# Kernel tuning notes

Measured on AMD Instinct MI355X. Metric: run time of the kernel, lower is better.

The kernel has to match this reference:

```python
import jax, jax.numpy as jnp
import numpy as np

B, CIN, COUT, H, W = 8, 64, 64, 56, 56
HEAD, KATT, KCONV = 1, 5, 3
HEAD_DIM = COUT // HEAD
PAD = (1 * (KATT - 1) + 1) // 2  # dilation=1 -> 2


def setup_inputs() -> dict:
    key = jax.random.key(0)
    ks = jax.random.split(key, 12)
    n = jax.random.normal
    return {
        'x': n(ks[0], (B, CIN, H, W), jnp.float32),
        'w1': n(ks[1], (COUT, CIN), jnp.float32) * 0.05,
        'b1': n(ks[2], (COUT,), jnp.float32) * 0.05,
        'w2': n(ks[3], (COUT, CIN), jnp.float32) * 0.05,
        'b2': n(ks[4], (COUT,), jnp.float32) * 0.05,
        'w3': n(ks[5], (COUT, CIN), jnp.float32) * 0.05,
        'b3': n(ks[6], (COUT,), jnp.float32) * 0.05,
        'wp': n(ks[7], (HEAD_DIM, 2), jnp.float32) * 0.05,
        'bp': n(ks[8], (HEAD_DIM,), jnp.float32) * 0.05,
        'w_fc': n(ks[9], (KCONV * KCONV, 3 * HEAD), jnp.float32) * 0.05,
        'w_dep': n(ks[10], (COUT, KCONV * KCONV, KCONV, KCONV), jnp.float32) * 0.05,
        'b_dep': n(ks[11], (COUT,), jnp.float32) * 0.05,
        'rate1': jnp.full((1,), 0.5, jnp.float32),
        'rate2': jnp.full((1,), 0.5, jnp.float32),
    }


def _conv1x1(x, w, b):
    return jnp.einsum('oc,bchw->bohw', w, x) + b[None, :, None, None]


def _unfold(x, h, w):
    # reflection-pad then extract KATTxKATT patches -> (n, c, KATT*KATT, h, w)
    p = jnp.pad(x, ((0, 0), (0, 0), (PAD, PAD), (PAD, PAD)), mode='reflect')
    return jnp.stack([p[:, :, i:i + h, j:j + w]
                      for i in range(KATT) for j in range(KATT)], axis=2)


def reference(x, w1, b1, w2, b2, w3, b3, wp, bp, w_fc, w_dep, b_dep, rate1, rate2):
    b, _, h, w = x.shape
    q = _conv1x1(x, w1, b1)
    k = _conv1x1(x, w2, b2)
    v = _conv1x1(x, w3, b3)
    head_dim = wp.shape[0]
    head = q.shape[1] // head_dim
    scaling = float(head_dim) ** -0.5

    # relative position embedding (stride=1 so q_pe == pe)
    loc_w = jnp.tile(jnp.linspace(-1.0, 1.0, w)[None, :], (h, 1))
    loc_h = jnp.tile(jnp.linspace(-1.0, 1.0, h)[:, None], (1, w))
    pe = _conv1x1(jnp.stack([loc_w, loc_h])[None], wp, bp)  # (1, head_dim, h, w)

    q_att = q.reshape(b * head, head_dim, h, w) * scaling
    k_att = k.reshape(b * head, head_dim, h, w)
    v_att = v.reshape(b * head, head_dim, h, w)

    unfold_k = _unfold(k_att, h, w)          # (b*head, d, 25, h, w)
    unfold_rpe = _unfold(pe, h, w)           # (1, d, 25, h, w)
    att = jnp.sum(q_att[:, :, None] * (unfold_k + pe[:, :, None] - unfold_rpe), axis=1)
    att = jax.nn.softmax(att, axis=1)        # softmax over the 25 window positions
    unfold_v = _unfold(v_att, h, w)
    out_att = jnp.sum(att[:, None] * unfold_v, axis=2).reshape(b, -1, h, w)

    # parallel depthwise-conv branch
    f_cat = jnp.concatenate([q.reshape(b, head, head_dim, h * w),
                             k.reshape(b, head, head_dim, h * w),
                             v.reshape(b, head, head_dim, h * w)], axis=1)  # (b, 3h, d, hw)
    f_all = jnp.einsum('oc,bcdl->bodl', w_fc, f_cat)                        # (b, 9, d, hw)
    f_conv = jnp.transpose(f_all, (0, 2, 1, 3)).reshape(b, head_dim * KCONV * KCONV, h, w)
    out_conv = jax.lax.conv_general_dilated(
        f_conv, w_dep, window_strides=(1, 1), padding=((1, 1), (1, 1)),
        feature_group_count=head_dim,
        dimension_numbers=('NCHW', 'OIHW', 'NCHW')) + b_dep[None, :, None, None]

    return rate1[0] * out_att + rate2[0] * out_conv
```

## Files before the change

kernel.cpp:

```cpp
#include <hip/hip_runtime.h>

#define HH 56
#define WWID 56
#define HWP (HH*WWID)
#define BB 8
#define CC 64
#define NPIX (BB*HWP)

__device__ __forceinline__ float grp_sum(float x) {
  int xi;
  xi = __builtin_amdgcn_update_dpp(0, __float_as_int(x), 0xB1, 0xF, 0xF, true);
  x += __int_as_float(xi);
  xi = __builtin_amdgcn_update_dpp(0, __float_as_int(x), 0x4E, 0xF, 0xF, true);
  x += __int_as_float(xi);
  xi = __builtin_amdgcn_update_dpp(0, __float_as_int(x), 0x141, 0xF, 0xF, true);
  x += __int_as_float(xi);
  xi = __builtin_amdgcn_update_dpp(0, __float_as_int(x), 0x140, 0xF, 0xF, true);
  x += __int_as_float(xi);
  return x;
}

__device__ __forceinline__ float dot4(float4 a, float4 b) {
  float t = a.x * b.x;
  t = fmaf(a.y, b.y, t);
  t = fmaf(a.z, b.z, t);
  t = fmaf(a.w, b.w, t);
  return t;
}

__device__ __forceinline__ float fcomp(const float4 v, int i) {
  return i == 0 ? v.x : i == 1 ? v.y : i == 2 ? v.z : v.w;
}

__global__ __launch_bounds__(256) void prep_kernel(
    const float* __restrict__ w1, const float* __restrict__ w2, const float* __restrict__ w3,
    const float* __restrict__ w_fc, const float* __restrict__ w_dep,
    float* __restrict__ w1P, float* __restrict__ w2P, float* __restrict__ w3P,
    float* __restrict__ tab)
{
  const int gt = blockIdx.x * 256 + threadIdx.x;
  {
    const int idx = gt;
    const int c4 = idx >> 8, r = idx & 255, o = r >> 2, e = r & 3;
    const int c = c4*4 + e;
    w1P[idx] = w1[o*64 + c];
    w2P[idx] = w2[o*64 + c];
    w3P[idx] = w3[o*64 + c];
  }
  if (gt < 27*64) {
    const int d = gt & 63, bt = gt >> 6;
    const int br = bt / 9, tap = bt - br*9;
    float s = 0.f;
    #pragma unroll
    for (int oo = 0; oo < 9; ++oo)
      s += w_dep[d*81 + oo*9 + tap] * w_fc[oo*3 + br];
    tab[gt] = s;
  }
}

__global__ __launch_bounds__(256) void qkv_kernel(
    const float* __restrict__ x,
    const float* __restrict__ b1, const float* __restrict__ b2, const float* __restrict__ b3,
    const float* __restrict__ w1P, const float* __restrict__ w2P, const float* __restrict__ w3P,
    float* __restrict__ q, float* __restrict__ k, float* __restrict__ v)
{
  __shared__ float xs[64 * 32];
  const int tid = threadIdx.x;

  int bid = (int)blockIdx.x;
  bid = (bid & 7) * 98 + (bid >> 3);

  const int pix0 = bid * 32;
  const int n    = pix0 / HWP;
  const int hw0  = pix0 - n * HWP;
  const float* xb = x + (size_t)n * CC * HWP + hw0;

  #pragma unroll
  for (int r = 0; r < 2; ++r) {
    int idx = r * 256 + tid;
    int c   = idx >> 3;
    int p4  = (idx & 7) * 4;
    *reinterpret_cast<float4*>(&xs[c*32 + p4]) =
        *reinterpret_cast<const float4*>(xb + (size_t)c * HWP + p4);
  }
  __syncthreads();

  const int o = tid & 63;
  const int g = __builtin_amdgcn_readfirstlane((int)(tid >> 6));
  const float* xg = &xs[g * 8];

  float accq[8], acck[8], accv[8];
  const float bq = b1[o], bk = b2[o], bv = b3[o];
  #pragma unroll
  for (int p = 0; p < 8; ++p) { accq[p] = bq; acck[p] = bk; accv[p] = bv; }

  float4 xbuf[2][4];
  float4 wqb[2], wkb[2], wvb[2];

  xbuf[0][0] = *reinterpret_cast<const float4*>(xg + 0*32);
  xbuf[0][1] = *reinterpret_cast<const float4*>(xg + 0*32 + 4);
  xbuf[0][2] = *reinterpret_cast<const float4*>(xg + 1*32);
  xbuf[0][3] = *reinterpret_cast<const float4*>(xg + 1*32 + 4);
  wqb[0] = *reinterpret_cast<const float4*>(w1P + o*4);
  wkb[0] = *reinterpret_cast<const float4*>(w2P + o*4);
  wvb[0] = *reinterpret_cast<const float4*>(w3P + o*4);

  #pragma unroll
  for (int ph = 0; ph < 32; ++ph) {
    const int cur  = ph & 1, nxt = cur ^ 1;
    const int c4   = ph >> 1;
    const int wsel = c4 & 1;
    if (ph < 31) {
      const int cn = (ph + 1) * 2;
      xbuf[nxt][0] = *reinterpret_cast<const float4*>(xg + (cn+0)*32);
      xbuf[nxt][1] = *reinterpret_cast<const float4*>(xg + (cn+0)*32 + 4);
      xbuf[nxt][2] = *reinterpret_cast<const float4*>(xg + (cn+1)*32);
      xbuf[nxt][3] = *reinterpret_cast<const float4*>(xg + (cn+1)*32 + 4);
    }
    if (cur == 0 && c4 < 15) {
      wqb[wsel^1] = *reinterpret_cast<const float4*>(w1P + (c4+1)*256 + o*4);
      wkb[wsel^1] = *reinterpret_cast<const float4*>(w2P + (c4+1)*256 + o*4);
      wvb[wsel^1] = *reinterpret_cast<const float4*>(w3P + (c4+1)*256 + o*4);
    }
    const float wq0 = fcomp(wqb[wsel], cur*2), wq1 = fcomp(wqb[wsel], cur*2+1);
    const float wk0 = fcomp(wkb[wsel], cur*2), wk1 = fcomp(wkb[wsel], cur*2+1);
    const float wv0 = fcomp(wvb[wsel], cur*2), wv1 = fcomp(wvb[wsel], cur*2+1);
    #pragma unroll
    for (int p = 0; p < 8; ++p) {
      const float x0 = (p < 4) ? fcomp(xbuf[cur][0], p) : fcomp(xbuf[cur][1], p-4);
      const float x1 = (p < 4) ? fcomp(xbuf[cur][2], p) : fcomp(xbuf[cur][3], p-4);
      accq[p] = fmaf(wq0, x0, accq[p]);
      acck[p] = fmaf(wk0, x0, acck[p]);
      accv[p] = fmaf(wv0, x0, accv[p]);
      accq[p] = fmaf(wq1, x1, accq[p]);
      acck[p] = fmaf(wk1, x1, acck[p]);
      accv[p] = fmaf(wv1, x1, accv[p]);
    }
  }

  const int pbase = pix0 + g * 8;
  #pragma unroll
  for (int p = 0; p < 8; ++p) {
    size_t off = (size_t)(pbase + p) * 64 + o;
    q[off] = accq[p]; k[off] = acck[p]; v[off] = accv[p];
  }
}

__global__ __launch_bounds__(256) void attn_kernel(
    const float* __restrict__ q, const float* __restrict__ k, const float* __restrict__ v,
    const float* __restrict__ wp, const float* __restrict__ tab,
    const float* __restrict__ b_dep, const float* __restrict__ rate1, const float* __restrict__ rate2,
    float* __restrict__ out)
{
  __shared__ float stab[27 * 64];
  __shared__ float sbd[64];
  __shared__ float sout[64 * 17];

  const int tid  = threadIdx.x;
  for (int i = tid; i < 27*64; i += 256) stab[i] = tab[i];
  if (tid < 64) sbd[tid] = b_dep[tid];
  __syncthreads();

  const int lane = tid & 63;
  const int wid  = __builtin_amdgcn_readfirstlane((int)(tid >> 6));
  const int grp  = lane >> 4;
  const int sl   = lane & 15;

  int bid = (int)blockIdx.x;
  bid = (bid & 7) * 196 + (bid >> 3);

  const int pixbase = bid * 16;
  const int pl  = wid * 4 + grp;
  const int pix = pixbase + pl;
  const int n   = pix / HWP;
  const int hw  = pix - n * HWP;
  const int h   = hw / WWID;
  const int w   = hw - h * WWID;

  const size_t nbase = (size_t)n * HWP * 64;
  const float4 q4 = *reinterpret_cast<const float4*>(q + nbase + (size_t)hw * 64 + sl * 4);

  int hr[5], wr[5];
  #pragma unroll
  for (int i = 0; i < 5; ++i) {
    int t = h + i - 2; hr[i] = t < 0 ? -t : (t >= HH ? 2*HH - 2 - t : t);
    t = w + i - 2;     wr[i] = t < 0 ? -t : (t >= WWID ? 2*WWID - 2 - t : t);
  }

  const float* kb = k + nbase + sl * 4;
  const float* vb = v + nbase + sl * 4;

  float4 ka[5], va[5];
  {
    const size_t rowoff = (size_t)(hr[0] * WWID) * 64;
    const float* krow = kb + rowoff;
    const float* vrow = vb + rowoff;
    #pragma unroll
    for (int j = 0; j < 5; ++j) ka[j] = *reinterpret_cast<const float4*>(krow + wr[j] * 64);
    #pragma unroll
    for (int j = 0; j < 5; ++j) va[j] = *reinterpret_cast<const float4*>(vrow + wr[j] * 64);
  }

  const float4 wa = *reinterpret_cast<const float4*>(wp + 8 * sl);
  const float4 wb = *reinterpret_cast<const float4*>(wp + 8 * sl + 4);
  const float4 wpx4 = {wa.x, wa.z, wb.x, wb.z};
  const float4 wpy4 = {wa.y, wa.w, wb.y, wb.w};
  const float qw0 = grp_sum(dot4(q4, wpx4));
  const float qw1 = grp_sum(dot4(q4, wpy4));

  const float LOG2E = 1.44269504f;
  const float L  = 0.125f * LOG2E;
  const float C  = 2.0f / 55.0f;
  const float A0 = L * qw0 * C;
  const float A1 = L * qw1 * C;

  float s = 0.f;
  float4 oatt = {0.f, 0.f, 0.f, 0.f};
  float4 cacc = {0.f, 0.f, 0.f, 0.f};

  #pragma unroll
  for (int i = 0; i < 5; ++i) {
    float4 kn[5], vn[5];
    if (i < 4) {
      const size_t rowoff = (size_t)(hr[i+1] * WWID) * 64;
      const float* krow = kb + rowoff;
      const float* vrow = vb + rowoff;
      #pragma unroll
      for (int j = 0; j < 5; ++j) kn[j] = *reinterpret_cast<const float4*>(krow + wr[j] * 64);
      #pragma unroll
      for (int j = 0; j < 5; ++j) vn[j] = *reinterpret_cast<const float4*>(vrow + wr[j] * 64);
    }

    const float rh = A1 * (float)(h - hr[i]);
    #pragma unroll
    for (int j = 0; j < 5; ++j) {
      const float d16 = grp_sum(dot4(q4, ka[j]));
      const float att = fmaf(L, d16, fmaf(A0, (float)(w - wr[j]), rh));
      const float p = __builtin_exp2f(att);
      s += p;
      oatt.x = fmaf(p, va[j].x, oatt.x);
      oatt.y = fmaf(p, va[j].y, oatt.y);
      oatt.z = fmaf(p, va[j].z, oatt.z);
      oatt.w = fmaf(p, va[j].w, oatt.w);
    }

    if (i >= 1 && i <= 3) {
      const int hh = h + i - 2;
      #pragma unroll
      for (int kw = 0; kw < 3; ++kw) {
        const int wc = w + kw - 1;
        const float mk = (((unsigned)hh < HH) && ((unsigned)wc < WWID)) ? 1.f : 0.f;
        const int tap = (i-1)*3 + kw;
        const int j = kw + 1;
        const float4 tq = *reinterpret_cast<const float4*>(&stab[(0*9 + tap)*64 + sl*4]);
        const float4 tk = *reinterpret_cast<const float4*>(&stab[(1*9 + tap)*64 + sl*4]);
        const float4 tv = *reinterpret_cast<const float4*>(&stab[(2*9 + tap)*64 + sl*4]);
        const float4 qn = *reinterpret_cast<const float4*>(q + nbase + (size_t)(hr[i]*WWID + wr[j]) * 64 + sl * 4);
        float sx = tq.x*qn.x; sx = fmaf(tk.x, ka[j].x, sx); sx = fmaf(tv.x, va[j].x, sx);
        float sy = tq.y*qn.y; sy = fmaf(tk.y, ka[j].y, sy); sy = fmaf(tv.y, va[j].y, sy);
        float sz = tq.z*qn.z; sz = fmaf(tk.z, ka[j].z, sz); sz = fmaf(tv.z, va[j].z, sz);
        float sw = tq.w*qn.w; sw = fmaf(tk.w, ka[j].w, sw); sw = fmaf(tv.w, va[j].w, sw);
        cacc.x = fmaf(mk, sx, cacc.x);
        cacc.y = fmaf(mk, sy, cacc.y);
        cacc.z = fmaf(mk, sz, cacc.z);
        cacc.w = fmaf(mk, sw, cacc.w);
      }
    }

    if (i < 4) {
      #pragma unroll
      for (int j = 0; j < 5; ++j) { ka[j] = kn[j]; va[j] = vn[j]; }
    }
  }

  const float inv = 1.0f / s;
  const float bdx = sbd[sl*4+0], bdy = sbd[sl*4+1], bdz = sbd[sl*4+2], bdw = sbd[sl*4+3];
  const float r1 = rate1[0] * inv;
  const float r2 = rate2[0];

  float res[4];
  res[0] = r1 * oatt.x + r2 * (cacc.x + bdx);
  res[1] = r1 * oatt.y + r2 * (cacc.y + bdy);
  res[2] = r1 * oatt.z + r2 * (cacc.z + bdz);
  res[3] = r1 * oatt.w + r2 * (cacc.w + bdw);

  #pragma unroll
  for (int e = 0; e < 4; ++e)
    sout[(4*sl + e)*17 + pl] = res[e];
  __syncthreads();

  const int c  = tid >> 2;
  const int e4 = (tid & 3) * 4;
  const int hw0 = pixbase - n * HWP;
  float4 o4 = {sout[c*17 + e4 + 0], sout[c*17 + e4 + 1],
               sout[c*17 + e4 + 2], sout[c*17 + e4 + 3]};
  *reinterpret_cast<float4*>(out + ((size_t)(n*64 + c))*HWP + hw0 + e4) = o4;
}

extern "C" void kernel_launch(void* const* d_in, const int* in_sizes, int n_in,
                              void* d_out, int out_size, void* d_ws, size_t ws_size,
                              hipStream_t stream) {
  const float* x     = (const float*)d_in[0];
  const float* w1    = (const float*)d_in[1];
  const float* b1    = (const float*)d_in[2];
  const float* w2    = (const float*)d_in[3];
  const float* b2    = (const float*)d_in[4];
  const float* w3    = (const float*)d_in[5];
  const float* b3    = (const float*)d_in[6];
  const float* wp    = (const float*)d_in[7];
  const float* w_fc  = (const float*)d_in[9];
  const float* w_dep = (const float*)d_in[10];
  const float* b_dep = (const float*)d_in[11];
  const float* rate1 = (const float*)d_in[12];
  const float* rate2 = (const float*)d_in[13];
  float* out = (float*)d_out;

  float* ws = (float*)d_ws;
  float* q   = ws;
  float* k   = ws + (size_t)NPIX*64;
  float* v   = ws + (size_t)2*NPIX*64;
  float* w1P = ws + (size_t)3*NPIX*64;
  float* w2P = w1P + 4096;
  float* w3P = w2P + 4096;
  float* tab = w3P + 4096;

  prep_kernel<<<16, 256, 0, stream>>>(w1, w2, w3, w_fc, w_dep, w1P, w2P, w3P, tab);
  qkv_kernel<<<NPIX/32, 256, 0, stream>>>(x, b1, b2, b3, w1P, w2P, w3P, q, k, v);
  attn_kernel<<<NPIX/16, 256, 0, stream>>>(q, k, v, wp, tab, b_dep, rate1, rate2, out);
}
```

Before: 42.55 us.

## Tile attention over 4x4 pixel blocks with shared-memory K/V/Q halos

The attention kernel now handles a 4x4 spatial tile per block instead of 16 consecutive pixels in a row. It first stages an 8x8 halo of K and V and a 6x6 halo of Q into LDS, and the 5x5 window and 3x3 conv gathers read from there. This replaces scattered global float4 loads with neighbour reuse inside the block. In exchange it uses much more LDS per block, which may cut occupancy, and the conv tap table and depthwise bias are now read from global memory rather than LDS. Reflection indices are mapped into the clamped halo, which stays valid because a reflected index always lands inside the tile's halo.

```diff
diff --git a/kernel.cpp b/kernel.cpp
--- a/kernel.cpp
+++ b/kernel.cpp
@@ -30,6 +30,10 @@
 
 __device__ __forceinline__ float fcomp(const float4 v, int i) {
   return i == 0 ? v.x : i == 1 ? v.y : i == 2 ? v.z : v.w;
+}
+
+__device__ __forceinline__ int clampi(int v, int lo, int hi) {
+  return v < lo ? lo : (v > hi ? hi : v);
 }
 
 __global__ __launch_bounds__(256) void prep_kernel(
@@ -152,53 +156,74 @@
     const float* __restrict__ b_dep, const float* __restrict__ rate1, const float* __restrict__ rate2,
     float* __restrict__ out)
 {
-  __shared__ float stab[27 * 64];
-  __shared__ float sbd[64];
+  __shared__ float kt[64 * 64];
+  __shared__ float vt[64 * 64];
+  __shared__ float qt[36 * 64];
   __shared__ float sout[64 * 17];
 
-  const int tid  = threadIdx.x;
-  for (int i = tid; i < 27*64; i += 256) stab[i] = tab[i];
-  if (tid < 64) sbd[tid] = b_dep[tid];
+  const int tid = threadIdx.x;
+
+  const int raw = (int)blockIdx.x;
+  const int n   = raw & 7;
+  const int t   = raw >> 3;
+  const int tr  = t / 14;
+  const int tc  = t - tr * 14;
+  const int t0  = tr * 4;
+  const int c0  = tc * 4;
+
+  const size_t nbase = (size_t)n * HWP * 64;
+
+  #pragma unroll
+  for (int rep = 0; rep < 4; ++rep) {
+    const int idx = rep * 256 + tid;
+    const int pos = idx >> 4;
+    const int f   = (idx & 15) * 4;
+    const int r   = pos >> 3, c = pos & 7;
+    const int gr  = clampi(t0 - 2 + r, 0, HH - 1);
+    const int gc  = clampi(c0 - 2 + c, 0, WWID - 1);
+    const size_t src = nbase + (size_t)(gr * WWID + gc) * 64 + f;
+    *reinterpret_cast<float4*>(&kt[pos * 64 + f]) = *reinterpret_cast<const float4*>(k + src);
+    *reinterpret_cast<float4*>(&vt[pos * 64 + f]) = *reinterpret_cast<const float4*>(v + src);
+  }
+  #pragma unroll
+  for (int rep = 0; rep < 3; ++rep) {
+    const int idx = rep * 256 + tid;
+    if (idx < 576) {
+      const int pos = idx >> 4;
+      const int f   = (idx & 15) * 4;
+      const int r   = pos / 6, c = pos - r * 6;
+      const int gr  = clampi(t0 - 1 + r, 0, HH - 1);
+      const int gc  = clampi(c0 - 1 + c, 0, WWID - 1);
+      *reinterpret_cast<float4*>(&qt[pos * 64 + f]) =
+          *reinterpret_cast<const float4*>(q + nbase + (size_t)(gr * WWID + gc) * 64 + f);
+    }
+  }
   __syncthreads();
 
-  const int lane = tid & 63;
-  const int wid  = __builtin_amdgcn_readfirstlane((int)(tid >> 6));
-  const int grp  = lane >> 4;
-  const int sl   = lane & 15;
-
-  int bid = (int)blockIdx.x;
-  bid = (bid & 7) * 196 + (bid >> 3);
-
-  const int pixbase = bid * 16;
-  const int pl  = wid * 4 + grp;
-  const int pix = pixbase + pl;
-  const int n   = pix / HWP;
-  const int hw  = pix - n * HWP;
-  const int h   = hw / WWID;
-  const int w   = hw - h * WWID;
-
-  const size_t nbase = (size_t)n * HWP * 64;
-  const float4 q4 = *reinterpret_cast<const float4*>(q + nbase + (size_t)hw * 64 + sl * 4);
-
-  int hr[5], wr[5];
+  const int group = tid >> 4;
+  const int sl    = tid & 15;
+  const int pr    = group >> 2;
+  const int pc    = group & 3;
+  const int h     = t0 + pr;
+  const int w     = c0 + pc;
+
+  const float4 q4 = *reinterpret_cast<const float4*>(&qt[((pr + 1) * 6 + (pc + 1)) * 64 + sl * 4]);
+
+  int kr[5], kc[5], hrg[5], wrg[5];
   #pragma unroll
   for (int i = 0; i < 5; ++i) {
-    int t = h + i - 2; hr[i] = t < 0 ? -t : (t >= HH ? 2*HH - 2 - t : t);
-    t = w + i - 2;     wr[i] = t < 0 ? -t : (t >= WWID ? 2*WWID - 2 - t : t);
-  }
-
-  const float* kb = k + nbase + sl * 4;
-  const float* vb = v + nbase + sl * 4;
+    int tt = h + i - 2; hrg[i] = tt < 0 ? -tt : (tt >= HH ? 2*HH - 2 - tt : tt);
+    kr[i] = hrg[i] - t0 + 2;
+    tt = w + i - 2;     wrg[i] = tt < 0 ? -tt : (tt >= WWID ? 2*WWID - 2 - tt : tt);
+    kc[i] = wrg[i] - c0 + 2;
+  }
 
   float4 ka[5], va[5];
-  {
-    const size_t rowoff = (size_t)(hr[0] * WWID) * 64;
-    const float* krow = kb + rowoff;
-    const float* vrow = vb + rowoff;
-    #pragma unroll
-    for (int j = 0; j < 5; ++j) ka[j] = *reinterpret_cast<const float4*>(krow + wr[j] * 64);
-    #pragma unroll
-    for (int j = 0; j < 5; ++j) va[j] = *reinterpret_cast<const float4*>(vrow + wr[j] * 64);
+  #pragma unroll
+  for (int j = 0; j < 5; ++j) {
+    const int p0 = (kr[0] * 8 + kc[j]) * 64 + sl * 4;
+    ka[j] = *reinterpret_cast<const float4*>(&kt[p0]);
+    va[j] = *reinterpret_cast<const float4*>(&vt[p0]);
   }
 
   const float4 wa = *reinterpret_cast<const float4*>(wp + 8 * sl);
@@ -222,20 +247,19 @@
   for (int i = 0; i < 5; ++i) {
     float4 kn[5], vn[5];
     if (i < 4) {
-      const size_t rowoff = (size_t)(hr[i+1] * WWID) * 64;
-      const float* krow = kb + rowoff;
-      const float* vrow = vb + rowoff;
       #pragma unroll
-      for (int j = 0; j < 5; ++j) kn[j] = *reinterpret_cast<const float4*>(krow + wr[j] * 64);
-      #pragma unroll
-      for (int j = 0; j < 5; ++j) vn[j] = *reinterpret_cast<const float4*>(vrow + wr[j] * 64);
-    }
-
-    const float rh = A1 * (float)(h - hr[i]);
+      for (int j = 0; j < 5; ++j) {
+        const int p1 = (kr[i+1] * 8 + kc[j]) * 64 + sl * 4;
+        kn[j] = *reinterpret_cast<const float4*>(&kt[p1]);
+        vn[j] = *reinterpret_cast<const float4*>(&vt[p1]);
+      }
+    }
+
+    const float rh = A1 * (float)(h - hrg[i]);
     #pragma unroll
     for (int j = 0; j < 5; ++j) {
       const float d16 = grp_sum(dot4(q4, ka[j]));
-      const float att = fmaf(L, d16, fmaf(A0, (float)(w - wr[j]), rh));
+      const float att = fmaf(L, d16, fmaf(A0, (float)(w - wrg[j]), rh));
       const float p = __builtin_exp2f(att);
       s += p;
       oatt.x = fmaf(p, va[j].x, oatt.x);
@@ -245,17 +269,18 @@
     }
 
     if (i >= 1 && i <= 3) {
-      const int hh = h + i - 2;
+      const int kh = i - 1;
+      const int hh = h + kh - 1;
       #pragma unroll
       for (int kw = 0; kw < 3; ++kw) {
         const int wc = w + kw - 1;
         const float mk = (((unsigned)hh < HH) && ((unsigned)wc < WWID)) ? 1.f : 0.f;
-        const int tap = (i-1)*3 + kw;
+        const int tap = kh*3 + kw;
         const int j = kw + 1;
-        const float4 tq = *reinterpret_cast<const float4*>(&stab[(0*9 + tap)*64 + sl*4]);
-        const float4 tk = *reinterpret_cast<const float4*>(&stab[(1*9 + tap)*64 + sl*4]);
-        const float4 tv = *reinterpret_cast<const float4*>(&stab[(2*9 + tap)*64 + sl*4]);
-        const float4 qn = *reinterpret_cast<const float4*>(q + nbase + (size_t)(hr[i]*WWID + wr[j]) * 64 + sl * 4);
+        const float4 tq = *reinterpret_cast<const float4*>(tab + (0*9 + tap)*64 + sl*4);
+        const float4 tk = *reinterpret_cast<const float4*>(tab + (1*9 + tap)*64 + sl*4);
+        const float4 tv = *reinterpret_cast<const float4*>(tab + (2*9 + tap)*64 + sl*4);
+        const float4 qn = *reinterpret_cast<const float4*>(&qt[((pr + kh) * 6 + (pc + kw)) * 64 + sl * 4]);
         float sx = tq.x*qn.x; sx = fmaf(tk.x, ka[j].x, sx); sx = fmaf(tv.x, va[j].x, sx);
         float sy = tq.y*qn.y; sy = fmaf(tk.y, ka[j].y, sy); sy = fmaf(tv.y, va[j].y, sy);
         float sz = tq.z*qn.z; sz = fmaf(tk.z, ka[j].z, sz); sz = fmaf(tv.z, va[j].z, sz);
@@ -274,27 +299,26 @@
   }
 
   const float inv = 1.0f / s;
-  const float bdx = sbd[sl*4+0], bdy = sbd[sl*4+1], bdz = sbd[sl*4+2], bdw = sbd[sl*4+3];
+  const float4 bd = *reinterpret_cast<const float4*>(b_dep + sl * 4);
   const float r1 = rate1[0] * inv;
   const float r2 = rate2[0];
 
   float res[4];
-  res[0] = r1 * oatt.x + r2 * (cacc.x + bdx);
-  res[1] = r1 * oatt.y + r2 * (cacc.y + bdy);
-  res[2] = r1 * oatt.z + r2 * (cacc.z + bdz);
-  res[3] = r1 * oatt.w + r2 * (cacc.w + bdw);
+  res[0] = r1 * oatt.x + r2 * (cacc.x + bd.x);
+  res[1] = r1 * oatt.y + r2 * (cacc.y + bd.y);
+  res[2] = r1 * oatt.z + r2 * (cacc.z + bd.z);
+  res[3] = r1 * oatt.w + r2 * (cacc.w + bd.w);
 
   #pragma unroll
   for (int e = 0; e < 4; ++e)
-    sout[(4*sl + e)*17 + pl] = res[e];
+    sout[(4*sl + e)*17 + group] = res[e];
   __syncthreads();
 
-  const int c  = tid >> 2;
-  const int e4 = (tid & 3) * 4;
-  const int hw0 = pixbase - n * HWP;
-  float4 o4 = {sout[c*17 + e4 + 0], sout[c*17 + e4 + 1],
-               sout[c*17 + e4 + 2], sout[c*17 + e4 + 3]};
-  *reinterpret_cast<float4*>(out + ((size_t)(n*64 + c))*HWP + hw0 + e4) = o4;
+  const int cc  = tid >> 2;
+  const int pr2 = tid & 3;
+  float4 o4 = {sout[cc*17 + pr2*4 + 0], sout[cc*17 + pr2*4 + 1],
+               sout[cc*17 + pr2*4 + 2], sout[cc*17 + pr2*4 + 3]};
+  *reinterpret_cast<float4*>(out + ((size_t)(n*64 + cc))*HWP + (t0 + pr2)*WWID + c0) = o4;
 }
 
 extern "C" void kernel_launch(void* const* d_in, const int* in_sizes, int n_in,
```

Result: no change. 41.89 us (-1.6%).
